# Kernel tuning notes

Hardware: AMD Instinct MI355X
Metric: run time of the kernel (lower is better)

## Reference

```python
import jax, jax.numpy as jnp
import numpy as np

E = 256  # embedding_dim
H = 256  # hidden_dim
B = 65536


def setup_inputs() -> dict:
    key = jax.random.key(0)
    ks = jax.random.split(key, 15)
    inp = {
        "x": jax.random.normal(ks[0], (B, E), dtype=jnp.float32),
        "c": jax.random.normal(ks[1], (B, H), dtype=jnp.float32),
        "h": jax.random.normal(ks[2], (B, H), dtype=jnp.float32),
    }
    names = ["W_i", "U_i", "b_i", "W_f", "U_f", "b_f", "W_c", "U_c", "b_c", "W_o", "U_o", "b_o"]
    shapes = [(E, H), (H, H), (H,)] * 4
    for n, s, k in zip(names, shapes, ks[3:]):
        inp[n] = jax.random.normal(k, s, dtype=jnp.float32)
    return inp


def reference(x, c, h, W_i, U_i, b_i, W_f, U_f, b_f, W_c, U_c, b_c, W_o, U_o, b_o):
    # Batch the four input/hidden projections into two GEMMs, then fuse gates.
    W = jnp.concatenate([W_f, W_i, W_o, W_c], axis=1)  # [E, 4H]
    U = jnp.concatenate([U_f, U_i, U_o, U_c], axis=1)  # [H, 4H]
    b = jnp.concatenate([b_f, b_i, b_o, b_c], axis=0)  # [4H]
    z = x @ W + h @ U + b                               # [B, 4H]
    zf, zi, zo, zg = jnp.split(z, 4, axis=1)
    f = jax.nn.sigmoid(zf)
    i = jax.nn.sigmoid(zi)
    o = jax.nn.sigmoid(zo)
    g = jnp.tanh(zg)
    c_new = c * f + g * i
    h_new = o * jnp.tanh(c_new)
    return (c_new, h_new)
```

## Files before the change

kernel.cpp:

```cpp
#include <hip/hip_runtime.h>
#include <hip/hip_fp16.h>

typedef _Float16 half8 __attribute__((ext_vector_type(8)));
typedef float f32x4 __attribute__((ext_vector_type(4)));

#define BHSZ 16777216
#define SLOT_BYTES 49152
#define B_OFF 32768

#define SBAR() __builtin_amdgcn_s_barrier()

__device__ __forceinline__ void gload16(const void* g, const void* lds) {
  __builtin_amdgcn_global_load_lds((const __attribute__((address_space(1))) void*)g,
                                   (__attribute__((address_space(3))) void*)lds,
                                   16, 0, 0);
}

__device__ __forceinline__ float fast_sigmoid(float z) {
  float e = __builtin_amdgcn_exp2f(-z * 1.4426950408889634f);
  return __builtin_amdgcn_rcpf(1.0f + e);
}

__device__ __forceinline__ float fast_tanh(float z) {
  float a = __builtin_fabsf(z);
  float e = __builtin_amdgcn_exp2f(a * 2.8853900817779268f);
  float t = 1.0f - 2.0f * __builtin_amdgcn_rcpf(1.0f + e);
  return z < 0.0f ? -t : t;
}

__global__ __launch_bounds__(256) void pack_b(
    const float* __restrict__ Wf, const float* __restrict__ Uf,
    const float* __restrict__ Wi, const float* __restrict__ Ui,
    const float* __restrict__ Wo, const float* __restrict__ Uo,
    const float* __restrict__ Wc, const float* __restrict__ Uc,
    _Float16* __restrict__ Bp) {
  int idx = blockIdx.x * 256 + threadIdx.x;
  int k = idx & 511;
  int Np = idx >> 9;
  int g = (Np >> 4) & 3;
  int cl = ((Np >> 6) << 4) | (Np & 15);
  const float* W;
  const float* U;
  switch (g) {
    case 0: W = Wf; U = Uf; break;
    case 1: W = Wi; U = Ui; break;
    case 2: W = Wo; U = Uo; break;
    default: W = Wc; U = Uc; break;
  }
  float v = (k < 256) ? W[k * 256 + cl] : U[(k - 256) * 256 + cl];
  Bp[idx] = (_Float16)v;
}

__global__ __launch_bounds__(512, 2) void lstm_fused(
    const float* __restrict__ x, const float* __restrict__ h,
    const _Float16* __restrict__ Bp, const float* __restrict__ cin,
    const float* __restrict__ bf_, const float* __restrict__ bi_,
    const float* __restrict__ bo_, const float* __restrict__ bc_,
    float* __restrict__ out) {
  extern __shared__ __align__(16) char smem[];

  int tid = threadIdx.x;
  int w = tid >> 6, l = tid & 63;
  int l15 = l & 15, lg = l >> 4;
  int wr = w >> 2, wcn = w & 3;

  int bid = blockIdx.x;
  int wg = (bid & 7) * 128 + (bid >> 3);
  int bm = wg >> 2, bn = wg & 3;

  int fA[4];
#pragma unroll
  for (int p = 0; p < 4; ++p) {
    int idx = p * 512 + tid;
    int r = idx >> 3, s = idx & 7;
    fA[p] = (bm * 256 + r) * 256 + ((s ^ (r & 7)) << 2);
  }
  int fB[2];
#pragma unroll
  for (int p = 0; p < 2; ++p) {
    int idx = p * 512 + tid;
    int r = idx >> 2, s = idx & 3;
    fB[p] = (bn * 256 + r) * 512 + ((s ^ (r & 3)) << 3);
  }
  int ldsA[4], ldsB[2];
#pragma unroll
  for (int p = 0; p < 4; ++p) ldsA[p] = (p * 512 + w * 64) * 16;
#pragma unroll
  for (int p = 0; p < 2; ++p) ldsB[p] = B_OFF + (p * 512 + w * 64) * 16;

  int offA[8][2], offB[4];
#pragma unroll
  for (int mf = 0; mf < 8; ++mf) {
    int r = wr * 128 + mf * 16 + l15;
#pragma unroll
    for (int b = 0; b < 2; ++b)
      offA[mf][b] = r * 128 + (((lg * 2 + b) ^ (r & 7)) << 4);
  }
#pragma unroll
  for (int nf = 0; nf < 4; ++nf) {
    int r = wcn * 64 + nf * 16 + l15;
    offB[nf] = B_OFF + r * 64 + ((lg ^ (r & 3)) << 4);
  }

  f32x4 acc[8][4];
#pragma unroll
  for (int a2 = 0; a2 < 8; ++a2)
#pragma unroll
    for (int b2 = 0; b2 < 4; ++b2)
      acc[a2][b2] = (f32x4){0.f, 0.f, 0.f, 0.f};

  auto stage = [&](int j2) {
    char* db = smem + (j2 % 3) * SLOT_BYTES;
    const float* srcA = (j2 < 8) ? x : h;
    int kbA = (j2 & 7) * 32;
#pragma unroll
    for (int p = 0; p < 4; ++p)
      gload16(srcA + fA[p] + kbA, db + ldsA[p] - B_OFF + B_OFF);
#pragma unroll
    for (int p = 0; p < 2; ++p)
      gload16(Bp + fB[p] + j2 * 32, db + ldsB[p]);
  };

  stage(0);
  stage(1);

#pragma unroll
  for (int j = 0; j < 16; ++j) {
    if (j == 15)
      asm volatile("s_waitcnt vmcnt(0)" ::: "memory");
    else
      asm volatile("s_waitcnt vmcnt(6)" ::: "memory");
    SBAR();
    if (j <= 13) stage(j + 2);

    const char* sb = smem + (j % 3) * SLOT_BYTES;
    half8 bv[4];
#pragma unroll
    for (int nf = 0; nf < 4; ++nf)
      bv[nf] = *reinterpret_cast<const half8*>(sb + offB[nf]);
#pragma unroll
    for (int bat = 0; bat < 2; ++bat) {
      f32x4 a0[4], a1[4];
#pragma unroll
      for (int q = 0; q < 4; ++q) {
        int mf = bat * 4 + q;
        a0[q] = *reinterpret_cast<const f32x4*>(sb + offA[mf][0]);
        a1[q] = *reinterpret_cast<const f32x4*>(sb + offA[mf][1]);
      }
      __builtin_amdgcn_s_setprio(1);
#pragma unroll
      for (int q = 0; q < 4; ++q) {
        int mf = bat * 4 + q;
        half8 av;
        av[0] = (_Float16)a0[q][0]; av[1] = (_Float16)a0[q][1];
        av[2] = (_Float16)a0[q][2]; av[3] = (_Float16)a0[q][3];
        av[4] = (_Float16)a1[q][0]; av[5] = (_Float16)a1[q][1];
        av[6] = (_Float16)a1[q][2]; av[7] = (_Float16)a1[q][3];
#pragma unroll
        for (int nf = 0; nf < 4; ++nf)
          acc[mf][nf] = __builtin_amdgcn_mfma_f32_16x16x32_f16(
              av, bv[nf], acc[mf][nf], 0, 0, 0);
      }
      __builtin_amdgcn_s_setprio(0);
    }
  }

  int col = (bn * 4 + wcn) * 16 + l15;
  float vbf = bf_[col], vbi = bi_[col], vbo = bo_[col], vbc = bc_[col];
#pragma unroll
  for (int mf = 0; mf < 8; ++mf) {
#pragma unroll
    for (int r = 0; r < 4; ++r) {
      long row = (long)(bm * 256 + wr * 128 + mf * 16 + lg * 4 + r);
      float zf = acc[mf][0][r] + vbf;
      float zi = acc[mf][1][r] + vbi;
      float zo = acc[mf][2][r] + vbo;
      float zg = acc[mf][3][r] + vbc;
      float fg = fast_sigmoid(zf);
      float ig = fast_sigmoid(zi);
      float og = fast_sigmoid(zo);
      float gg = fast_tanh(zg);
      float cv = cin[row * 256 + col];
      float cn = cv * fg + gg * ig;
      float hn = og * fast_tanh(cn);
      out[row * 256 + col] = cn;
      out[BHSZ + row * 256 + col] = hn;
    }
  }
}

extern "C" void kernel_launch(void* const* d_in, const int* in_sizes, int n_in,
                              void* d_out, int out_size, void* d_ws, size_t ws_size,
                              hipStream_t stream) {
  const float* x  = (const float*)d_in[0];
  const float* c  = (const float*)d_in[1];
  const float* h  = (const float*)d_in[2];
  const float* Wi = (const float*)d_in[3];
  const float* Ui = (const float*)d_in[4];
  const float* bi = (const float*)d_in[5];
  const float* Wf = (const float*)d_in[6];
  const float* Uf = (const float*)d_in[7];
  const float* bf = (const float*)d_in[8];
  const float* Wc = (const float*)d_in[9];
  const float* Uc = (const float*)d_in[10];
  const float* bc = (const float*)d_in[11];
  const float* Wo = (const float*)d_in[12];
  const float* Uo = (const float*)d_in[13];
  const float* bo = (const float*)d_in[14];

  _Float16* Bp = (_Float16*)d_ws;

  pack_b<<<2048, 256, 0, stream>>>(Wf, Uf, Wi, Ui, Wo, Uo, Wc, Uc, Bp);
  lstm_fused<<<1024, 512, 3 * SLOT_BYTES, stream>>>(x, h, Bp, c, bf, bi, bo,
                                                    bc, (float*)d_out);
}
```

Before: 139.3 us.

## Shrink GEMM tiles to 128x128 with 4-wave blocks and 4096 workgroups

Reduces the block tile from 256x256 (8 waves) to 128x128 (4 waves), halving LDS per slot and quadrupling the grid. The B-tile LDS layout is repacked so two rows share one 128-byte swizzled line, and a sched_barrier is added at the end of each K iteration. The aim is higher occupancy, a smaller tail effect and less register pressure per wave, but each block now does less data reuse, so more global and L2 traffic is needed for the A and B tiles.

New measurement: 177.4 us. 27.4% more time.

```diff
diff --git a/kernel.cpp b/kernel.cpp
--- a/kernel.cpp
+++ b/kernel.cpp
@@ -5,10 +5,10 @@
 typedef float f32x4 __attribute__((ext_vector_type(4)));
 
 #define BHSZ 16777216
-#define SLOT_BYTES 49152
-#define B_OFF 32768
-
+#define SLOT_BYTES 24576
+#define B_OFF 16384
 #define SBAR() __builtin_amdgcn_s_barrier()
+#define SCHEDB() __builtin_amdgcn_sched_barrier(0)
 
 __device__ __forceinline__ void gload16(const void* g, const void* lds) {
   __builtin_amdgcn_global_load_lds((const __attribute__((address_space(1))) void*)g,
@@ -51,7 +51,7 @@
   Bp[idx] = (_Float16)v;
 }
 
-__global__ __launch_bounds__(512, 2) void lstm_fused(
+__global__ __launch_bounds__(256, 2) void lstm_fused(
     const float* __restrict__ x, const float* __restrict__ h,
     const _Float16* __restrict__ Bp, const float* __restrict__ cin,
     const float* __restrict__ bf_, const float* __restrict__ bi_,
@@ -62,36 +62,38 @@
   int tid = threadIdx.x;
   int w = tid >> 6, l = tid & 63;
   int l15 = l & 15, lg = l >> 4;
-  int wr = w >> 2, wcn = w & 3;
+  int wr = w >> 1, wcn = w & 1;
 
   int bid = blockIdx.x;
-  int wg = (bid & 7) * 128 + (bid >> 3);
-  int bm = wg >> 2, bn = wg & 3;
+  int wg = (bid & 7) * 512 + (bid >> 3);
+  int bm = wg >> 3, bn = wg & 7;
 
   int fA[4];
 #pragma unroll
   for (int p = 0; p < 4; ++p) {
-    int idx = p * 512 + tid;
+    int idx = p * 256 + tid;
     int r = idx >> 3, s = idx & 7;
-    fA[p] = (bm * 256 + r) * 256 + ((s ^ (r & 7)) << 2);
+    fA[p] = (bm * 128 + r) * 256 + ((s ^ (r & 7)) << 2);
   }
   int fB[2];
 #pragma unroll
   for (int p = 0; p < 2; ++p) {
-    int idx = p * 512 + tid;
-    int r = idx >> 2, s = idx & 3;
-    fB[p] = (bn * 256 + r) * 512 + ((s ^ (r & 3)) << 3);
+    int d = p * 256 + tid;
+    int rp = d >> 3, s8 = d & 7;
+    int i8 = s8 ^ (rp & 7);
+    int r = rp * 2 + (i8 >> 2), c = i8 & 3;
+    fB[p] = (bn * 128 + r) * 512 + (c << 3);
   }
   int ldsA[4], ldsB[2];
 #pragma unroll
-  for (int p = 0; p < 4; ++p) ldsA[p] = (p * 512 + w * 64) * 16;
-#pragma unroll
-  for (int p = 0; p < 2; ++p) ldsB[p] = B_OFF + (p * 512 + w * 64) * 16;
-
-  int offA[8][2], offB[4];
-#pragma unroll
-  for (int mf = 0; mf < 8; ++mf) {
-    int r = wr * 128 + mf * 16 + l15;
+  for (int p = 0; p < 4; ++p) ldsA[p] = (p * 256 + w * 64) * 16;
+#pragma unroll
+  for (int p = 0; p < 2; ++p) ldsB[p] = B_OFF + (p * 256 + w * 64) * 16;
+
+  int offA[4][2], offB[4];
+#pragma unroll
+  for (int mf = 0; mf < 4; ++mf) {
+    int r = wr * 64 + mf * 16 + l15;
 #pragma unroll
     for (int b = 0; b < 2; ++b)
       offA[mf][b] = r * 128 + (((lg * 2 + b) ^ (r & 7)) << 4);
@@ -99,26 +101,25 @@
 #pragma unroll
   for (int nf = 0; nf < 4; ++nf) {
     int r = wcn * 64 + nf * 16 + l15;
-    offB[nf] = B_OFF + r * 64 + ((lg ^ (r & 3)) << 4);
-  }
-
-  f32x4 acc[8][4];
-#pragma unroll
-  for (int a2 = 0; a2 < 8; ++a2)
+    int rp = r >> 1;
+    offB[nf] = B_OFF + rp * 128 + (((((r & 1) << 2) | lg) ^ (rp & 7)) << 4);
+  }
+
+  f32x4 acc[4][4];
+#pragma unroll
+  for (int a2 = 0; a2 < 4; ++a2)
 #pragma unroll
     for (int b2 = 0; b2 < 4; ++b2)
       acc[a2][b2] = (f32x4){0.f, 0.f, 0.f, 0.f};
 
   auto stage = [&](int j2) {
     char* db = smem + (j2 % 3) * SLOT_BYTES;
-    const float* srcA = (j2 < 8) ? x : h;
-    int kbA = (j2 & 7) * 32;
-#pragma unroll
-    for (int p = 0; p < 4; ++p)
-      gload16(srcA + fA[p] + kbA, db + ldsA[p] - B_OFF + B_OFF);
-#pragma unroll
-    for (int p = 0; p < 2; ++p)
-      gload16(Bp + fB[p] + j2 * 32, db + ldsB[p]);
+    const float* sa = (j2 < 8) ? x : h;
+    int kb = (j2 & 7) * 32;
+#pragma unroll
+    for (int p = 0; p < 4; ++p) gload16(sa + fA[p] + kb, db + ldsA[p]);
+#pragma unroll
+    for (int p = 0; p < 2; ++p) gload16(Bp + fB[p] + j2 * 32, db + ldsB[p]);
   };
 
   stage(0);
@@ -138,40 +139,36 @@
 #pragma unroll
     for (int nf = 0; nf < 4; ++nf)
       bv[nf] = *reinterpret_cast<const half8*>(sb + offB[nf]);
-#pragma unroll
-    for (int bat = 0; bat < 2; ++bat) {
-      f32x4 a0[4], a1[4];
-#pragma unroll
-      for (int q = 0; q < 4; ++q) {
-        int mf = bat * 4 + q;
-        a0[q] = *reinterpret_cast<const f32x4*>(sb + offA[mf][0]);
-        a1[q] = *reinterpret_cast<const f32x4*>(sb + offA[mf][1]);
-      }
-      __builtin_amdgcn_s_setprio(1);
-#pragma unroll
-      for (int q = 0; q < 4; ++q) {
-        int mf = bat * 4 + q;
-        half8 av;
-        av[0] = (_Float16)a0[q][0]; av[1] = (_Float16)a0[q][1];
-        av[2] = (_Float16)a0[q][2]; av[3] = (_Float16)a0[q][3];
-        av[4] = (_Float16)a1[q][0]; av[5] = (_Float16)a1[q][1];
-        av[6] = (_Float16)a1[q][2]; av[7] = (_Float16)a1[q][3];
-#pragma unroll
-        for (int nf = 0; nf < 4; ++nf)
-          acc[mf][nf] = __builtin_amdgcn_mfma_f32_16x16x32_f16(
-              av, bv[nf], acc[mf][nf], 0, 0, 0);
-      }
-      __builtin_amdgcn_s_setprio(0);
+    f32x4 a0[4], a1[4];
+#pragma unroll
+    for (int mf = 0; mf < 4; ++mf) {
+      a0[mf] = *reinterpret_cast<const f32x4*>(sb + offA[mf][0]);
+      a1[mf] = *reinterpret_cast<const f32x4*>(sb + offA[mf][1]);
     }
-  }
-
-  int col = (bn * 4 + wcn) * 16 + l15;
+    __builtin_amdgcn_s_setprio(1);
+#pragma unroll
+    for (int mf = 0; mf < 4; ++mf) {
+      half8 av;
+      av[0] = (_Float16)a0[mf][0]; av[1] = (_Float16)a0[mf][1];
+      av[2] = (_Float16)a0[mf][2]; av[3] = (_Float16)a0[mf][3];
+      av[4] = (_Float16)a1[mf][0]; av[5] = (_Float16)a1[mf][1];
+      av[6] = (_Float16)a1[mf][2]; av[7] = (_Float16)a1[mf][3];
+#pragma unroll
+      for (int nf = 0; nf < 4; ++nf)
+        acc[mf][nf] = __builtin_amdgcn_mfma_f32_16x16x32_f16(
+            av, bv[nf], acc[mf][nf], 0, 0, 0);
+    }
+    __builtin_amdgcn_s_setprio(0);
+    SCHEDB();
+  }
+
+  int col = (bn * 2 + wcn) * 16 + l15;
   float vbf = bf_[col], vbi = bi_[col], vbo = bo_[col], vbc = bc_[col];
 #pragma unroll
-  for (int mf = 0; mf < 8; ++mf) {
+  for (int mf = 0; mf < 4; ++mf) {
 #pragma unroll
     for (int r = 0; r < 4; ++r) {
-      long row = (long)(bm * 256 + wr * 128 + mf * 16 + lg * 4 + r);
+      long row = (long)(bm * 128 + wr * 64 + mf * 16 + lg * 4 + r);
       float zf = acc[mf][0][r] + vbf;
       float zi = acc[mf][1][r] + vbi;
       float zo = acc[mf][2][r] + vbo;
@@ -211,6 +208,6 @@
   _Float16* Bp = (_Float16*)d_ws;
 
   pack_b<<<2048, 256, 0, stream>>>(Wf, Uf, Wi, Ui, Wo, Uo, Wc, Uc, Bp);
-  lstm_fused<<<1024, 512, 3 * SLOT_BYTES, stream>>>(x, h, Bp, c, bf, bi, bo,
+  lstm_fused<<<4096, 256, 3 * SLOT_BYTES, stream>>>(x, h, Bp, c, bf, bi, bo,
                                                     bc, (float*)d_out);
 }
```

## Stage A through registers, convert to fp16 before LDS write

Applied to the files above, without the earlier changes.

A tiles are no longer copied straight from global memory into LDS as fp32. Each thread now loads them into registers, converts them to fp16, and writes them to LDS in a new paired-row swizzled layout, which halves A's LDS footprint and slot size. The MFMA inner loop then reads half8 fragments directly and drops the per-iteration fp32-to-fp16 conversions and the doubled LDS reads. The cost is extra VGPRs for the register staging and an lgkmcnt wait plus a register round-trip in the pipeline, which may reduce latency hiding.

New measurement: 149.1 us. 7.1% more time.

```diff
diff --git a/kernel.cpp b/kernel.cpp
--- a/kernel.cpp
+++ b/kernel.cpp
@@ -2,13 +2,14 @@
 #include <hip/hip_fp16.h>
 
 typedef _Float16 half8 __attribute__((ext_vector_type(8)));
+typedef _Float16 half4 __attribute__((ext_vector_type(4)));
 typedef float f32x4 __attribute__((ext_vector_type(4)));
 
 #define BHSZ 16777216
-#define SLOT_BYTES 49152
-#define B_OFF 32768
-
+#define SLOT_BYTES 32768
+#define B_OFF 16384
 #define SBAR() __builtin_amdgcn_s_barrier()
+#define WAITL() asm volatile("s_waitcnt lgkmcnt(0)" ::: "memory")
 
 __device__ __forceinline__ void gload16(const void* g, const void* lds) {
   __builtin_amdgcn_global_load_lds((const __attribute__((address_space(1))) void*)g,
@@ -68,38 +69,42 @@
   int wg = (bid & 7) * 128 + (bid >> 3);
   int bm = wg >> 2, bn = wg & 3;
 
-  int fA[4];
+  int aRowLo = tid >> 3;
+  int aKpos = (tid & 7) * 4;
+  int aWoff[4];
 #pragma unroll
   for (int p = 0; p < 4; ++p) {
-    int idx = p * 512 + tid;
-    int r = idx >> 3, s = idx & 7;
-    fA[p] = (bm * 256 + r) * 256 + ((s ^ (r & 7)) << 2);
-  }
+    int row = p * 64 + aRowLo;
+    int rp = row >> 1;
+    int c = ((((row & 1) << 2) | (aKpos >> 3)) ^ (rp & 7));
+    aWoff[p] = rp * 128 + (c << 4) + ((tid & 1) << 3);
+  }
+
   int fB[2];
 #pragma unroll
   for (int p = 0; p < 2; ++p) {
-    int idx = p * 512 + tid;
-    int r = idx >> 2, s = idx & 3;
-    fB[p] = (bn * 256 + r) * 512 + ((s ^ (r & 3)) << 3);
-  }
-  int ldsA[4], ldsB[2];
-#pragma unroll
-  for (int p = 0; p < 4; ++p) ldsA[p] = (p * 512 + w * 64) * 16;
+    int d = p * 512 + tid;
+    int rp = d >> 3, s8 = d & 7;
+    int i8 = s8 ^ (rp & 7);
+    int r = rp * 2 + (i8 >> 2), cb = i8 & 3;
+    fB[p] = (bn * 256 + r) * 512 + (cb << 3);
+  }
+  int ldsB[2];
 #pragma unroll
   for (int p = 0; p < 2; ++p) ldsB[p] = B_OFF + (p * 512 + w * 64) * 16;
 
-  int offA[8][2], offB[4];
+  int offA[8], offB[4];
 #pragma unroll
   for (int mf = 0; mf < 8; ++mf) {
     int r = wr * 128 + mf * 16 + l15;
-#pragma unroll
-    for (int b = 0; b < 2; ++b)
-      offA[mf][b] = r * 128 + (((lg * 2 + b) ^ (r & 7)) << 4);
+    int rp = r >> 1;
+    offA[mf] = rp * 128 + (((((r & 1) << 2) | lg) ^ (rp & 7)) << 4);
   }
 #pragma unroll
   for (int nf = 0; nf < 4; ++nf) {
     int r = wcn * 64 + nf * 16 + l15;
-    offB[nf] = B_OFF + r * 64 + ((lg ^ (r & 3)) << 4);
+    int rp = r >> 1;
+    offB[nf] = B_OFF + rp * 128 + (((((r & 1) << 2) | lg) ^ (rp & 7)) << 4);
   }
 
   f32x4 acc[8][4];
@@ -109,29 +114,52 @@
     for (int b2 = 0; b2 < 4; ++b2)
       acc[a2][b2] = (f32x4){0.f, 0.f, 0.f, 0.f};
 
-  auto stage = [&](int j2) {
-    char* db = smem + (j2 % 3) * SLOT_BYTES;
-    const float* srcA = (j2 < 8) ? x : h;
-    int kbA = (j2 & 7) * 32;
-#pragma unroll
-    for (int p = 0; p < 4; ++p)
-      gload16(srcA + fA[p] + kbA, db + ldsA[p] - B_OFF + B_OFF);
+  f32x4 aReg[4];
+
+  auto issueA = [&](int t) {
+    const float* src = (t < 8) ? x : h;
+    int kb = (t & 7) * 32;
+#pragma unroll
+    for (int p = 0; p < 4; ++p) {
+      long row = (long)(bm * 256 + p * 64 + aRowLo);
+      aReg[p] = *reinterpret_cast<const f32x4*>(src + row * 256 + kb + aKpos);
+    }
+  };
+  auto issueB = [&](int t) {
+    char* db = smem + (t % 3) * SLOT_BYTES;
 #pragma unroll
     for (int p = 0; p < 2; ++p)
-      gload16(Bp + fB[p] + j2 * 32, db + ldsB[p]);
+      gload16(Bp + fB[p] + t * 32, db + ldsB[p]);
   };
-
-  stage(0);
-  stage(1);
+  auto writeA = [&](int t) {
+    char* db = smem + (t % 3) * SLOT_BYTES;
+#pragma unroll
+    for (int p = 0; p < 4; ++p) {
+      half4 o;
+      o[0] = (_Float16)aReg[p][0]; o[1] = (_Float16)aReg[p][1];
+      o[2] = (_Float16)aReg[p][2]; o[3] = (_Float16)aReg[p][3];
+      *reinterpret_cast<half4*>(db + aWoff[p]) = o;
+    }
+  };
+
+  issueB(0);
+  issueA(0);
+  asm volatile("s_waitcnt vmcnt(0)" ::: "memory");
+  writeA(0);
+  issueA(1);
+  issueB(1);
 
 #pragma unroll
   for (int j = 0; j < 16; ++j) {
     if (j == 15)
       asm volatile("s_waitcnt vmcnt(0)" ::: "memory");
     else
-      asm volatile("s_waitcnt vmcnt(6)" ::: "memory");
+      asm volatile("s_waitcnt vmcnt(2)" ::: "memory");
+    WAITL();
     SBAR();
-    if (j <= 13) stage(j + 2);
+    if (j <= 14) writeA(j + 1);
+    if (j <= 13) issueA(j + 2);
+    if (j <= 13) issueB(j + 2);
 
     const char* sb = smem + (j % 3) * SLOT_BYTES;
     half8 bv[4];
@@ -140,27 +168,17 @@
       bv[nf] = *reinterpret_cast<const half8*>(sb + offB[nf]);
 #pragma unroll
     for (int bat = 0; bat < 2; ++bat) {
-      f32x4 a0[4], a1[4];
-#pragma unroll
-      for (int q = 0; q < 4; ++q) {
-        int mf = bat * 4 + q;
-        a0[q] = *reinterpret_cast<const f32x4*>(sb + offA[mf][0]);
-        a1[q] = *reinterpret_cast<const f32x4*>(sb + offA[mf][1]);
-      }
+      half8 av[4];
+#pragma unroll
+      for (int q = 0; q < 4; ++q)
+        av[q] = *reinterpret_cast<const half8*>(sb + offA[bat * 4 + q]);
       __builtin_amdgcn_s_setprio(1);
 #pragma unroll
-      for (int q = 0; q < 4; ++q) {
-        int mf = bat * 4 + q;
-        half8 av;
-        av[0] = (_Float16)a0[q][0]; av[1] = (_Float16)a0[q][1];
-        av[2] = (_Float16)a0[q][2]; av[3] = (_Float16)a0[q][3];
-        av[4] = (_Float16)a1[q][0]; av[5] = (_Float16)a1[q][1];
-        av[6] = (_Float16)a1[q][2]; av[7] = (_Float16)a1[q][3];
+      for (int q = 0; q < 4; ++q)
 #pragma unroll
         for (int nf = 0; nf < 4; ++nf)
-          acc[mf][nf] = __builtin_amdgcn_mfma_f32_16x16x32_f16(
-              av, bv[nf], acc[mf][nf], 0, 0, 0);
-      }
+          acc[bat * 4 + q][nf] = __builtin_amdgcn_mfma_f32_16x16x32_f16(
+              av[q], bv[nf], acc[bat * 4 + q][nf], 0, 0, 0);
       __builtin_amdgcn_s_setprio(0);
     }
   }
```
